# Kernel optimization log

Hardware: AMD Instinct MI355X
Metric: run time of the kernel (lower is better)

## Reference

```python
import jax, jax.numpy as jnp
import numpy as np

N = 50000
E = 1600000
SI, SO, VI, VO, H, SVOD = 128, 128, 16, 16, 16, 3
EPS = 1e-8


def _safe_norm(x, axis, keepdims=False):
    return jnp.sqrt(jnp.sum(x * x, axis=axis, keepdims=keepdims) + EPS)


def setup_inputs() -> dict:
    key = jax.random.key(0)
    ks = jax.random.split(key, 13)

    def lin(k, fan_in, shape):
        b = 1.0 / np.sqrt(fan_in)
        return jax.random.uniform(k, shape, jnp.float32, -b, b)

    merged_dim = H + SI + 3 * SVOD  # 153
    return {
        "s": jax.random.normal(ks[0], (N, SI), jnp.float32),
        "v": jax.random.normal(ks[1], (N, VI, 3), jnp.float32),
        "frames": jax.random.normal(ks[2], (E, 3, 3), jnp.float32),
        "W_vd": lin(ks[3], VI, (VI, H)),            # vector_down (no bias)
        "W_vdf": lin(ks[4], VI, (VI, SVOD)),        # vector_down_frames (no bias)
        "W_so": lin(ks[5], merged_dim, (merged_dim, SO)),  # scalar_out
        "b_so": lin(ks[6], merged_dim, (SO,)),
        "W_vu": lin(ks[7], H, (H, VO)),             # vector_up (no bias)
        "W_vosf": lin(ks[8], SO, (SO, 3 * SVOD)),   # vector_out_scale_frames
        "b_vosf": lin(ks[9], SO, (3 * SVOD,)),
        "W_vuf": lin(ks[10], SVOD, (SVOD, VO)),     # vector_up_frames (no bias)
        "edge_index": jax.random.randint(ks[11], (2, E), 0, N, jnp.int32),
        "node_inputs": 1,
    }


def reference(s, v, frames, W_vd, W_vdf, W_so, b_so, W_vu, W_vosf, b_vosf, W_vuf, edge_index, node_inputs):
    # node_inputs is assumed truthy (node-wise GCP): gather by source node, scatter-mean back.
    row = edge_index[0]
    deg = jax.ops.segment_sum(jnp.ones((E,), s.dtype), row, num_segments=N)
    inv_deg = 1.0 / jnp.maximum(deg, 1.0)

    v_pre = jnp.swapaxes(v, -1, -2)                 # [N, 3, VI]
    vh = v_pre @ W_vd                                # [N, 3, H]
    vnorm = _safe_norm(vh, axis=-2)                  # [N, H]
    vdf = v_pre @ W_vdf                              # [N, 3, SVOD]

    # scalarize: project gathered source-node vectors onto per-edge frames, scatter-mean
    local = jnp.einsum('eij,ejc->eic', frames, vdf[row])       # [E, 3, SVOD]
    local9 = jnp.swapaxes(local, -1, -2).reshape(E, 3 * SVOD)  # [E, 9]
    sh = jax.ops.segment_sum(local9, row, num_segments=N) * inv_deg[:, None]  # [N, 9]

    merged = jnp.concatenate([s, vnorm, sh], axis=-1)          # [N, SI+H+9]
    scalar_rep = merged @ W_so + b_so                           # [N, SO]

    # vector path with frame gate
    vr = jnp.swapaxes(vh @ W_vu, -1, -2)                        # [N, VO, 3]
    gate = jax.nn.sigmoid(scalar_rep) @ W_vosf + b_vosf         # [N, 9]
    # vectorize: expand gate scalars back into vectors via frames, scatter-mean
    g = gate[row].reshape(E, 3, 3)
    gv_e = jnp.einsum('eji,ejk->eik', g, frames)                # [E, 3, 3]
    gv = jax.ops.segment_sum(gv_e, row, num_segments=N) * inv_deg[:, None, None]  # [N, 3, 3]
    gvr = jnp.swapaxes(jnp.swapaxes(gv, -1, -2) @ W_vuf, -1, -2)  # [N, VO, 3]
    vr = vr * jax.nn.sigmoid(_safe_norm(gvr, axis=-1, keepdims=True))

    return jax.nn.relu(scalar_rep), vr
```

## Files before the change

### kernel.cpp

```cpp
#include <hip/hip_runtime.h>

#define N_NODES 50000
#define N_EDGES 1600000
#define NPB     16
#define NCHAIN  16
#define KSTR    168
#define EPSV    1e-8f

typedef float f32x4 __attribute__((ext_vector_type(4)));
typedef short s16x8 __attribute__((ext_vector_type(8)));

struct f4u { float a, b, c, d; };

__device__ __forceinline__ float sigmoidf_(float x) { return 1.0f / (1.0f + __expf(-x)); }
__device__ __forceinline__ short f2bf(float x) {
    unsigned u = __float_as_uint(x);
    unsigned r = (u + 0x7FFFu + ((u >> 16) & 1u)) >> 16;
    return (short)r;
}
__device__ __forceinline__ float bf2f(short h) {
    return __uint_as_float(((unsigned)(unsigned short)h) << 16);
}

__global__ __launch_bounds__(256) void init_kernel(
    const float* __restrict__ W_so, short* __restrict__ WThi, short* __restrict__ WTlo,
    int* __restrict__ p0, int* __restrict__ p1, int mode) {
    int i = blockIdx.x * 256 + threadIdx.x;
    if (i < 128 * 160) {
        int o = i / 160, k = i - o * 160;
        float w = (k < 153) ? W_so[k * 128 + o] : 0.0f;
        short hh = f2bf(w);
        WThi[i] = hh;
        WTlo[i] = f2bf(w - bf2f(hh));
    }
    if (mode == 2) {
        if (i < N_NODES) p0[i] = 0;
        if (i < N_NODES * NCHAIN) p1[i] = -1;
    } else {
        if (i < N_NODES * NCHAIN) p0[i] = -1;
    }
}

__global__ __launch_bounds__(256) void bucket_csr_kernel(
    const int* __restrict__ row,
    const float* __restrict__ frames,
    int* __restrict__ cnt,
    int* __restrict__ head2,
    int* __restrict__ nxt_ovf,
    float* __restrict__ pay,
    int cap) {
    int e = blockIdx.x * 256 + threadIdx.x;
    if (e >= N_EDGES) return;
    int r = row[e];
    int lidx = atomicAdd(&cnt[r], 1);
    if (lidx < cap) {
        const float* f = frames + (size_t)e * 9;
        f4u x = ((const f4u*)f)[0];
        f4u y = ((const f4u*)f)[1];
        float z8 = f[8];
        float* dst = pay + ((size_t)r * cap + lidx) * 12;
        *(float4*)dst       = make_float4(x.a, x.b, x.c, x.d);
        *(float4*)(dst + 4) = make_float4(y.a, y.b, y.c, y.d);
        *(float4*)(dst + 8) = make_float4(z8, 0.0f, 0.0f, 0.0f);
    } else {
        int prev = atomicExch(&head2[r * NCHAIN + (e & (NCHAIN - 1))], e);
        nxt_ovf[e] = prev;
    }
}

__global__ __launch_bounds__(256) void bucket_fat_kernel(
    const int* __restrict__ row,
    const float* __restrict__ frames,
    int* __restrict__ head,
    float* __restrict__ pay) {
    int e = blockIdx.x * 256 + threadIdx.x;
    if (e >= N_EDGES) return;
    int r = row[e];
    int prev = atomicExch(&head[r * NCHAIN + (e & (NCHAIN - 1))], e);
    const float* f = frames + (size_t)e * 9;
    f4u x = ((const f4u*)f)[0];
    f4u y = ((const f4u*)f)[1];
    float z8 = f[8];
    float4* dst = (float4*)(pay + (size_t)e * 16);
    dst[0] = make_float4(x.a, x.b, x.c, x.d);
    dst[1] = make_float4(y.a, y.b, y.c, y.d);
    dst[2] = make_float4(z8, __int_as_float(prev), 0.0f, 0.0f);
}

__global__ __launch_bounds__(256) void bucket_thin_kernel(
    const int* __restrict__ row,
    int* __restrict__ head,
    int* __restrict__ nxt) {
    int e = blockIdx.x * 256 + threadIdx.x;
    if (e >= N_EDGES) return;
    int r = row[e];
    int prev = atomicExch(&head[r * NCHAIN + (e & (NCHAIN - 1))], e);
    nxt[e] = prev;
}

template<int MODE>
__global__ __launch_bounds__(256) void node_kernel(
    const float* __restrict__ s,
    const float* __restrict__ v,
    const float* __restrict__ fr,
    const float* __restrict__ frames_raw,
    const float* __restrict__ W_vd,
    const float* __restrict__ W_vdf,
    const short* __restrict__ WThi,
    const short* __restrict__ WTlo,
    const float* __restrict__ b_so,
    const float* __restrict__ W_vu,
    const float* __restrict__ W_vosf,
    const float* __restrict__ b_vosf,
    const float* __restrict__ W_vuf,
    const int* __restrict__ cnt_or_head,
    const int* __restrict__ head2,
    const int* __restrict__ nxt,
    int cap,
    float* __restrict__ out0,
    float* __restrict__ out1)
{
    __shared__ __align__(16) short AL[2][NPB][KSTR];
    __shared__ float vL[NPB][48];
    __shared__ float vhL[NPB][3][16];
    __shared__ float FbarL[NPB][9];
    __shared__ float gateL[NPB][12];

    float (*sigL)[128] = (float (*)[128])&AL[0][0][0];

    const int t = threadIdx.x;
    const int base = blockIdx.x * NPB;
    const int nn = t >> 4, h = t & 15;
    const int n = base + nn;

    int e0;
    if (MODE == 2) e0 = cnt_or_head[n];
    else           e0 = cnt_or_head[(size_t)n * NCHAIN + h];

#pragma unroll
    for (int r = 0; r < 3; r++) vL[nn][h * 3 + r] = v[(size_t)n * 48 + h * 3 + r];
    {
        const float4* sp4 = (const float4*)(s + (size_t)n * 128 + h * 8);
        float4 s0 = sp4[0], s1 = sp4[1];
        float sv[8] = {s0.x, s0.y, s0.z, s0.w, s1.x, s1.y, s1.z, s1.w};
        s16x8 shi, slo;
#pragma unroll
        for (int j = 0; j < 8; j++) {
            short hh = f2bf(sv[j]);
            shi[j] = hh;
            slo[j] = f2bf(sv[j] - bf2f(hh));
        }
        *(s16x8*)&AL[0][nn][h * 8] = shi;
        *(s16x8*)&AL[1][nn][h * 8] = slo;
    }

    float fs[10];
#pragma unroll
    for (int k = 0; k < 10; k++) fs[k] = 0.f;
    float invdeg;
    {
        if (MODE == 2) {
            const int cn = e0;
            const int lim = cn < cap ? cn : cap;
            for (int slot = h; slot < lim; slot += 16) {
                const float* pp = fr + ((size_t)n * cap + slot) * 12;
                float4 c0 = *(const float4*)pp;
                float4 c1 = *(const float4*)(pp + 4);
                float f8 = pp[8];
                fs[0] += c0.x; fs[1] += c0.y; fs[2] += c0.z; fs[3] += c0.w;
                fs[4] += c1.x; fs[5] += c1.y; fs[6] += c1.z; fs[7] += c1.w;
                fs[8] += f8;
            }
            int e2 = head2[(size_t)n * NCHAIN + h];
            while (e2 >= 0) {
                int en = nxt[e2];
                const float* f = frames_raw + (size_t)e2 * 9;
                f4u x = ((const f4u*)f)[0];
                f4u y = ((const f4u*)f)[1];
                float z8 = f[8];
                fs[0] += x.a; fs[1] += x.b; fs[2] += x.c; fs[3] += x.d;
                fs[4] += y.a; fs[5] += y.b; fs[6] += y.c; fs[7] += y.d;
                fs[8] += z8;
                e2 = en;
            }
#pragma unroll
            for (int m = 1; m < 16; m <<= 1) {
#pragma unroll
                for (int k = 0; k < 9; k++) fs[k] += __shfl_xor(fs[k], m);
            }
            invdeg = 1.0f / fmaxf((float)cn, 1.0f);
        } else if (MODE == 1) {
            int e = e0;
            while (e >= 0) {
                const float4* p = (const float4*)(fr + (size_t)e * 16);
                float4 c2 = p[2];
                float4 c0 = p[0];
                float4 c1 = p[1];
                int en = __float_as_int(c2.y);
                fs[0] += c0.x; fs[1] += c0.y; fs[2] += c0.z; fs[3] += c0.w;
                fs[4] += c1.x; fs[5] += c1.y; fs[6] += c1.z; fs[7] += c1.w;
                fs[8] += c2.x;
                fs[9] += 1.0f;
                e = en;
            }
#pragma unroll
            for (int m = 1; m < 16; m <<= 1) {
#pragma unroll
                for (int k = 0; k < 10; k++) fs[k] += __shfl_xor(fs[k], m);
            }
            invdeg = 1.0f / fmaxf(fs[9], 1.0f);
        } else {
            int e = e0;
            while (e >= 0) {
                int en = nxt[e];
                const float* f = fr + (size_t)e * 9;
                f4u x = ((const f4u*)f)[0];
                f4u y = ((const f4u*)f)[1];
                float z8 = f[8];
                fs[0] += x.a; fs[1] += x.b; fs[2] += x.c; fs[3] += x.d;
                fs[4] += y.a; fs[5] += y.b; fs[6] += y.c; fs[7] += y.d;
                fs[8] += z8;
                fs[9] += 1.0f;
                e = en;
            }
#pragma unroll
            for (int m = 1; m < 16; m <<= 1) {
#pragma unroll
                for (int k = 0; k < 10; k++) fs[k] += __shfl_xor(fs[k], m);
            }
            invdeg = 1.0f / fmaxf(fs[9], 1.0f);
        }
        if (h < 9) FbarL[nn][h] = fs[h] * invdeg;
    }
    __syncthreads();

    {
        float vh0 = 0.f, vh1 = 0.f, vh2 = 0.f;
#pragma unroll
        for (int i = 0; i < 16; i++) {
            float w = W_vd[i * 16 + h];
            vh0 += vL[nn][i * 3 + 0] * w;
            vh1 += vL[nn][i * 3 + 1] * w;
            vh2 += vL[nn][i * 3 + 2] * w;
        }
        vhL[nn][0][h] = vh0; vhL[nn][1][h] = vh1; vhL[nn][2][h] = vh2;
        float vn = sqrtf(vh0 * vh0 + vh1 * vh1 + vh2 * vh2 + EPSV);
        short hh = f2bf(vn);
        AL[0][nn][128 + h] = hh;
        AL[1][nn][128 + h] = f2bf(vn - bf2f(hh));
        if (h < 9) {
            const int c = h / 3, i = h % 3;
            float a = 0.f;
#pragma unroll
            for (int j = 0; j < 3; j++) {
                float vd = 0.f;
#pragma unroll
                for (int ii = 0; ii < 16; ii++) vd += vL[nn][ii * 3 + j] * W_vdf[ii * 3 + c];
                a += (fs[i * 3 + j] * invdeg) * vd;
            }
            short hs = f2bf(a);
            AL[0][nn][144 + h] = hs;
            AL[1][nn][144 + h] = f2bf(a - bf2f(hs));
        } else {
            AL[0][nn][144 + h] = 0;
            AL[1][nn][144 + h] = 0;
        }
    }
    __syncthreads();

    {
        const int w = t >> 6;
        const int lane = t & 63;
        const int quad = lane >> 4;
        const int col = lane & 15;
        const int o0 = w * 32 + col, o1 = o0 + 16;
        f32x4 acc0 = (f32x4){0.f, 0.f, 0.f, 0.f};
        f32x4 acc1 = (f32x4){0.f, 0.f, 0.f, 0.f};
#pragma unroll
        for (int kk = 0; kk < 5; kk++) {
            const int krow = kk * 32 + quad * 8;
            s16x8 ahi = *(const s16x8*)&AL[0][col][krow];
            s16x8 alo = *(const s16x8*)&AL[1][col][krow];
            s16x8 b0h = *(const s16x8*)&WThi[o0 * 160 + krow];
            s16x8 b0l = *(const s16x8*)&WTlo[o0 * 160 + krow];
            s16x8 b1h = *(const s16x8*)&WThi[o1 * 160 + krow];
            s16x8 b1l = *(const s16x8*)&WTlo[o1 * 160 + krow];
            acc0 = __builtin_amdgcn_mfma_f32_16x16x32_bf16(ahi, b0h, acc0, 0, 0, 0);
            acc0 = __builtin_amdgcn_mfma_f32_16x16x32_bf16(ahi, b0l, acc0, 0, 0, 0);
            acc0 = __builtin_amdgcn_mfma_f32_16x16x32_bf16(alo, b0h, acc0, 0, 0, 0);
            acc1 = __builtin_amdgcn_mfma_f32_16x16x32_bf16(ahi, b1h, acc1, 0, 0, 0);
            acc1 = __builtin_amdgcn_mfma_f32_16x16x32_bf16(ahi, b1l, acc1, 0, 0, 0);
            acc1 = __builtin_amdgcn_mfma_f32_16x16x32_bf16(alo, b1h, acc1, 0, 0, 0);
        }
        __syncthreads();
        {
            float b0 = b_so[o0], b1 = b_so[o1];
#pragma unroll
            for (int r = 0; r < 4; r++) {
                int nl = quad * 4 + r;
                float v0 = acc0[r] + b0;
                float v1 = acc1[r] + b1;
                out0[(size_t)(base + nl) * 128 + o0] = fmaxf(v0, 0.0f);
                out0[(size_t)(base + nl) * 128 + o1] = fmaxf(v1, 0.0f);
                sigL[nl][o0] = sigmoidf_(v0);
                sigL[nl][o1] = sigmoidf_(v1);
            }
        }
    }
    __syncthreads();

    {
        const float* sp = &sigL[nn][h * 8];
        float4 s0 = *(const float4*)sp;
        float4 s1 = *(const float4*)(sp + 4);
        float sv[8] = {s0.x, s0.y, s0.z, s0.w, s1.x, s1.y, s1.z, s1.w};
        float p[9];
#pragma unroll
        for (int k = 0; k < 9; k++) p[k] = 0.f;
#pragma unroll
        for (int i = 0; i < 8; i++) {
            int o = h * 8 + i;
#pragma unroll
            for (int k = 0; k < 9; k++) p[k] += sv[i] * W_vosf[o * 9 + k];
        }
#pragma unroll
        for (int m = 1; m < 16; m <<= 1) {
#pragma unroll
            for (int k = 0; k < 9; k++) p[k] += __shfl_xor(p[k], m);
        }
        if (h < 9) gateL[nn][h] = p[h] + b_vosf[h];
    }
    __syncthreads();

    {
        int o = h;
        float gv[9];
#pragma unroll
        for (int i = 0; i < 3; i++)
#pragma unroll
            for (int kk = 0; kk < 3; kk++) {
                float a = 0.f;
#pragma unroll
                for (int j = 0; j < 3; j++) a += gateL[nn][j * 3 + i] * FbarL[nn][j * 3 + kk];
                gv[i * 3 + kk] = a;
            }
        float gvr[3];
#pragma unroll
        for (int kk = 0; kk < 3; kk++) {
            float a = 0.f;
#pragma unroll
            for (int i = 0; i < 3; i++) a += gv[i * 3 + kk] * W_vuf[i * 16 + o];
            gvr[kk] = a;
        }
        float gn2 = sqrtf(gvr[0] * gvr[0] + gvr[1] * gvr[1] + gvr[2] * gvr[2] + EPSV);
        float sg = sigmoidf_(gn2);
#pragma unroll
        for (int c = 0; c < 3; c++) {
            float a = 0.f;
#pragma unroll
            for (int h2 = 0; h2 < 16; h2++) a += vhL[nn][c][h2] * W_vu[h2 * 16 + o];
            out1[(size_t)n * 48 + o * 3 + c] = a * sg;
        }
    }
}

extern "C" void kernel_launch(void* const* d_in, const int* in_sizes, int n_in,
                              void* d_out, int out_size, void* d_ws, size_t ws_size,
                              hipStream_t stream) {
    const float* s      = (const float*)d_in[0];
    const float* v      = (const float*)d_in[1];
    const float* frames = (const float*)d_in[2];
    const float* W_vd   = (const float*)d_in[3];
    const float* W_vdf  = (const float*)d_in[4];
    const float* W_so   = (const float*)d_in[5];
    const float* b_so   = (const float*)d_in[6];
    const float* W_vu   = (const float*)d_in[7];
    const float* W_vosf = (const float*)d_in[8];
    const float* b_vosf = (const float*)d_in[9];
    const float* W_vuf  = (const float*)d_in[10];
    const int* edge_index = (const int*)d_in[11];

    float* out0 = (float*)d_out;
    float* out1 = out0 + (size_t)N_NODES * 128;

    const size_t wt_b    = (size_t)128 * 160 * sizeof(short);
    const size_t cnt_b   = (size_t)N_NODES * sizeof(int);
    const size_t head2_b = (size_t)N_NODES * NCHAIN * sizeof(int);
    const size_t novf_b  = (size_t)N_EDGES * sizeof(int);
    const size_t csr_base = cnt_b + head2_b + 2 * wt_b + novf_b;
    long cap = 0;
    if (ws_size > csr_base)
        cap = (long)((ws_size - csr_base) / ((size_t)N_NODES * 48));
    if (cap > 64) cap = 64;

    const size_t head_b  = (size_t)N_NODES * NCHAIN * sizeof(int);
    const size_t fat_off = head_b + 2 * wt_b;
    const size_t fat_need = fat_off + (size_t)N_EDGES * 64;

    if (cap >= 32) {
        int*   cnt   = (int*)d_ws;
        int*   head2 = (int*)((char*)d_ws + cnt_b);
        short* WThi  = (short*)((char*)d_ws + cnt_b + head2_b);
        short* WTlo  = WThi + 128 * 160;
        int*   novf  = (int*)((char*)d_ws + cnt_b + head2_b + 2 * wt_b);
        float* pay   = (float*)((char*)d_ws + csr_base);
        init_kernel<<<(N_NODES * NCHAIN + 255) / 256, 256, 0, stream>>>(
            W_so, WThi, WTlo, cnt, head2, 2);
        bucket_csr_kernel<<<(N_EDGES + 255) / 256, 256, 0, stream>>>(
            edge_index, frames, cnt, head2, novf, pay, (int)cap);
        node_kernel<2><<<N_NODES / NPB, 256, 0, stream>>>(
            s, v, pay, frames, W_vd, W_vdf, WThi, WTlo, b_so, W_vu, W_vosf, b_vosf, W_vuf,
            cnt, head2, novf, (int)cap, out0, out1);
    } else if (ws_size >= fat_need) {
        int*   head = (int*)d_ws;
        short* WThi = (short*)((char*)d_ws + head_b);
        short* WTlo = WThi + 128 * 160;
        float* pay  = (float*)((char*)d_ws + fat_off);
        init_kernel<<<(N_NODES * NCHAIN + 255) / 256, 256, 0, stream>>>(
            W_so, WThi, WTlo, head, (int*)nullptr, 1);
        bucket_fat_kernel<<<(N_EDGES + 255) / 256, 256, 0, stream>>>(
            edge_index, frames, head, pay);
        node_kernel<1><<<N_NODES / NPB, 256, 0, stream>>>(
            s, v, pay, frames, W_vd, W_vdf, WThi, WTlo, b_so, W_vu, W_vosf, b_vosf, W_vuf,
            head, (const int*)nullptr, (const int*)nullptr, 0, out0, out1);
    } else {
        int*   head = (int*)d_ws;
        short* WThi = (short*)((char*)d_ws + head_b);
        short* WTlo = WThi + 128 * 160;
        int*   nxt  = (int*)((char*)d_ws + fat_off);
        init_kernel<<<(N_NODES * NCHAIN + 255) / 256, 256, 0, stream>>>(
            W_so, WThi, WTlo, head, (int*)nullptr, 1);
        bucket_thin_kernel<<<(N_EDGES + 255) / 256, 256, 0, stream>>>(
            edge_index, head, nxt);
        node_kernel<0><<<N_NODES / NPB, 256, 0, stream>>>(
            s, v, frames, frames, W_vd, W_vdf, WThi, WTlo, b_so, W_vu, W_vosf, b_vosf, W_vuf,
            head, (const int*)nullptr, nxt, 0, out0, out1);
    }
}
```

Before: 307.5 us.

## Bucket edges by 16-node bins instead of per-node CSR slots

Replaces the per-node bucketed payload (cap slots per node) with per-block bins of 16 nodes, where each edge stores its frame plus a local node id. The node kernel then reads its bin in one contiguous sweep across all 256 threads and reduces into shared memory with LDS float atomics. The goal is to cut atomic contention spread, lower per-node padding waste and uneven per-lane load, and get coalesced reads of the payload. In exchange it adds shared-memory atomics (ten per edge) and a bin-overflow linked-list fallback, and summation order becomes nondeterministic.

Measured after the change: 396.4 us. +28.9%, slower.

```diff
diff --git a/kernel.cpp b/kernel.cpp
--- a/kernel.cpp
+++ b/kernel.cpp
@@ -3,6 +3,7 @@
 #define N_NODES 50000
 #define N_EDGES 1600000
 #define NPB     16
+#define NBINS   (N_NODES / NPB)
 #define NCHAIN  16
 #define KSTR    168
 #define EPSV    1e-8f
@@ -33,38 +34,40 @@
         WThi[i] = hh;
         WTlo[i] = f2bf(w - bf2f(hh));
     }
-    if (mode == 2) {
-        if (i < N_NODES) p0[i] = 0;
+    if (mode == 3) {
+        if (i < NBINS) p0[i] = 0;
         if (i < N_NODES * NCHAIN) p1[i] = -1;
     } else {
         if (i < N_NODES * NCHAIN) p0[i] = -1;
     }
 }
 
-__global__ __launch_bounds__(256) void bucket_csr_kernel(
+__global__ __launch_bounds__(256) void bucket_bin_kernel(
     const int* __restrict__ row,
     const float* __restrict__ frames,
-    int* __restrict__ cnt,
+    int* __restrict__ bincnt,
     int* __restrict__ head2,
-    int* __restrict__ nxt_ovf,
+    int* __restrict__ nxt,
     float* __restrict__ pay,
     int cap) {
     int e = blockIdx.x * 256 + threadIdx.x;
     if (e >= N_EDGES) return;
     int r = row[e];
-    int lidx = atomicAdd(&cnt[r], 1);
-    if (lidx < cap) {
-        const float* f = frames + (size_t)e * 9;
-        f4u x = ((const f4u*)f)[0];
-        f4u y = ((const f4u*)f)[1];
-        float z8 = f[8];
-        float* dst = pay + ((size_t)r * cap + lidx) * 12;
-        *(float4*)dst       = make_float4(x.a, x.b, x.c, x.d);
-        *(float4*)(dst + 4) = make_float4(y.a, y.b, y.c, y.d);
-        *(float4*)(dst + 8) = make_float4(z8, 0.0f, 0.0f, 0.0f);
+    int b = r >> 4;
+    int slot = atomicAdd(&bincnt[b], 1);
+    const float* f = frames + (size_t)e * 9;
+    f4u x = ((const f4u*)f)[0];
+    f4u y = ((const f4u*)f)[1];
+    float z8 = f[8];
+    if (slot < cap) {
+        float* dst = pay + ((size_t)b * cap + slot) * 12;
+        ((f4u*)dst)[0] = x;
+        ((f4u*)dst)[1] = y;
+        dst[8] = z8;
+        ((int*)dst)[9] = r & (NPB - 1);
     } else {
         int prev = atomicExch(&head2[r * NCHAIN + (e & (NCHAIN - 1))], e);
-        nxt_ovf[e] = prev;
+        nxt[e] = prev;
     }
 }
 
@@ -98,11 +101,10 @@
     nxt[e] = prev;
 }
 
-template<int MODE>
-__global__ __launch_bounds__(256) void node_kernel(
+__global__ __launch_bounds__(256) void node_bin_kernel(
     const float* __restrict__ s,
     const float* __restrict__ v,
-    const float* __restrict__ fr,
+    const float* __restrict__ pay,
     const float* __restrict__ frames_raw,
     const float* __restrict__ W_vd,
     const float* __restrict__ W_vdf,
@@ -113,7 +115,7 @@
     const float* __restrict__ W_vosf,
     const float* __restrict__ b_vosf,
     const float* __restrict__ W_vuf,
-    const int* __restrict__ cnt_or_head,
+    const int* __restrict__ bincnt,
     const int* __restrict__ head2,
     const int* __restrict__ nxt,
     int cap,
@@ -125,6 +127,7 @@
     __shared__ float vhL[NPB][3][16];
     __shared__ float FbarL[NPB][9];
     __shared__ float gateL[NPB][12];
+    __shared__ float FsumL[NPB][10];
 
     float (*sigL)[128] = (float (*)[128])&AL[0][0][0];
 
@@ -133,10 +136,7 @@
     const int nn = t >> 4, h = t & 15;
     const int n = base + nn;
 
-    int e0;
-    if (MODE == 2) e0 = cnt_or_head[n];
-    else           e0 = cnt_or_head[(size_t)n * NCHAIN + h];
-
+    if (t < NPB * 10) ((float*)FsumL)[t] = 0.0f;
 #pragma unroll
     for (int r = 0; r < 3; r++) vL[nn][h * 3 + r] = v[(size_t)n * 48 + h * 3 + r];
     {
@@ -153,44 +153,235 @@
         *(s16x8*)&AL[0][nn][h * 8] = shi;
         *(s16x8*)&AL[1][nn][h * 8] = slo;
     }
+    __syncthreads();
+
+    {
+        int cn = bincnt[blockIdx.x];
+        int lim = cn < cap ? cn : cap;
+        for (int slot = t; slot < lim; slot += 256) {
+            const float* pp = pay + ((size_t)blockIdx.x * cap + slot) * 12;
+            f4u c0 = ((const f4u*)pp)[0];
+            f4u c1 = ((const f4u*)pp)[1];
+            float f8 = pp[8];
+            int nid = ((const int*)pp)[9];
+            float* Fs = FsumL[nid];
+            atomicAdd(&Fs[0], c0.a); atomicAdd(&Fs[1], c0.b);
+            atomicAdd(&Fs[2], c0.c); atomicAdd(&Fs[3], c0.d);
+            atomicAdd(&Fs[4], c1.a); atomicAdd(&Fs[5], c1.b);
+            atomicAdd(&Fs[6], c1.c); atomicAdd(&Fs[7], c1.d);
+            atomicAdd(&Fs[8], f8);   atomicAdd(&Fs[9], 1.0f);
+        }
+        int e2 = head2[(size_t)n * NCHAIN + h];
+        while (e2 >= 0) {
+            int en = nxt[e2];
+            const float* f = frames_raw + (size_t)e2 * 9;
+            f4u x = ((const f4u*)f)[0];
+            f4u y = ((const f4u*)f)[1];
+            float z8 = f[8];
+            float* Fs = FsumL[nn];
+            atomicAdd(&Fs[0], x.a); atomicAdd(&Fs[1], x.b);
+            atomicAdd(&Fs[2], x.c); atomicAdd(&Fs[3], x.d);
+            atomicAdd(&Fs[4], y.a); atomicAdd(&Fs[5], y.b);
+            atomicAdd(&Fs[6], y.c); atomicAdd(&Fs[7], y.d);
+            atomicAdd(&Fs[8], z8);  atomicAdd(&Fs[9], 1.0f);
+            e2 = en;
+        }
+    }
+    __syncthreads();
+
+    {
+        float fs[10];
+#pragma unroll
+        for (int k = 0; k < 10; k++) fs[k] = FsumL[nn][k];
+        float invdeg = 1.0f / fmaxf(fs[9], 1.0f);
+        if (h < 9) FbarL[nn][h] = fs[h] * invdeg;
+
+        float vh0 = 0.f, vh1 = 0.f, vh2 = 0.f;
+#pragma unroll
+        for (int i = 0; i < 16; i++) {
+            float w = W_vd[i * 16 + h];
+            vh0 += vL[nn][i * 3 + 0] * w;
+            vh1 += vL[nn][i * 3 + 1] * w;
+            vh2 += vL[nn][i * 3 + 2] * w;
+        }
+        vhL[nn][0][h] = vh0; vhL[nn][1][h] = vh1; vhL[nn][2][h] = vh2;
+        float vn = sqrtf(vh0 * vh0 + vh1 * vh1 + vh2 * vh2 + EPSV);
+        short hh = f2bf(vn);
+        AL[0][nn][128 + h] = hh;
+        AL[1][nn][128 + h] = f2bf(vn - bf2f(hh));
+        if (h < 9) {
+            const int c = h / 3, i = h % 3;
+            float a = 0.f;
+#pragma unroll
+            for (int j = 0; j < 3; j++) {
+                float vd = 0.f;
+#pragma unroll
+                for (int ii = 0; ii < 16; ii++) vd += vL[nn][ii * 3 + j] * W_vdf[ii * 3 + c];
+                a += (fs[i * 3 + j] * invdeg) * vd;
+            }
+            short hs = f2bf(a);
+            AL[0][nn][144 + h] = hs;
+            AL[1][nn][144 + h] = f2bf(a - bf2f(hs));
+        } else {
+            AL[0][nn][144 + h] = 0;
+            AL[1][nn][144 + h] = 0;
+        }
+    }
+    __syncthreads();
+
+    {
+        const int w = t >> 6;
+        const int lane = t & 63;
+        const int quad = lane >> 4;
+        const int col = lane & 15;
+        const int o0 = w * 32 + col, o1 = o0 + 16;
+        f32x4 acc0 = (f32x4){0.f, 0.f, 0.f, 0.f};
+        f32x4 acc1 = (f32x4){0.f, 0.f, 0.f, 0.f};
+#pragma unroll
+        for (int kk = 0; kk < 5; kk++) {
+            const int krow = kk * 32 + quad * 8;
+            s16x8 ahi = *(const s16x8*)&AL[0][col][krow];
+            s16x8 alo = *(const s16x8*)&AL[1][col][krow];
+            s16x8 b0h = *(const s16x8*)&WThi[o0 * 160 + krow];
+            s16x8 b0l = *(const s16x8*)&WTlo[o0 * 160 + krow];
+            s16x8 b1h = *(const s16x8*)&WThi[o1 * 160 + krow];
+            s16x8 b1l = *(const s16x8*)&WTlo[o1 * 160 + krow];
+            acc0 = __builtin_amdgcn_mfma_f32_16x16x32_bf16(ahi, b0h, acc0, 0, 0, 0);
+            acc0 = __builtin_amdgcn_mfma_f32_16x16x32_bf16(ahi, b0l, acc0, 0, 0, 0);
+            acc0 = __builtin_amdgcn_mfma_f32_16x16x32_bf16(alo, b0h, acc0, 0, 0, 0);
+            acc1 = __builtin_amdgcn_mfma_f32_16x16x32_bf16(ahi, b1h, acc1, 0, 0, 0);
+            acc1 = __builtin_amdgcn_mfma_f32_16x16x32_bf16(ahi, b1l, acc1, 0, 0, 0);
+            acc1 = __builtin_amdgcn_mfma_f32_16x16x32_bf16(alo, b1h, acc1, 0, 0, 0);
+        }
+        __syncthreads();
+        {
+            float b0 = b_so[o0], b1 = b_so[o1];
+#pragma unroll
+            for (int r = 0; r < 4; r++) {
+                int nl = quad * 4 + r;
+                float v0 = acc0[r] + b0;
+                float v1 = acc1[r] + b1;
+                out0[(size_t)(base + nl) * 128 + o0] = fmaxf(v0, 0.0f);
+                out0[(size_t)(base + nl) * 128 + o1] = fmaxf(v1, 0.0f);
+                sigL[nl][o0] = sigmoidf_(v0);
+                sigL[nl][o1] = sigmoidf_(v1);
+            }
+        }
+    }
+    __syncthreads();
+
+    {
+        const float* sp = &sigL[nn][h * 8];
+        float4 s0 = *(const float4*)sp;
+        float4 s1 = *(const float4*)(sp + 4);
+        float sv[8] = {s0.x, s0.y, s0.z, s0.w, s1.x, s1.y, s1.z, s1.w};
+        float p[9];
+#pragma unroll
+        for (int k = 0; k < 9; k++) p[k] = 0.f;
+#pragma unroll
+        for (int i = 0; i < 8; i++) {
+            int o = h * 8 + i;
+#pragma unroll
+            for (int k = 0; k < 9; k++) p[k] += sv[i] * W_vosf[o * 9 + k];
+        }
+#pragma unroll
+        for (int m = 1; m < 16; m <<= 1) {
+#pragma unroll
+            for (int k = 0; k < 9; k++) p[k] += __shfl_xor(p[k], m);
+        }
+        if (h < 9) gateL[nn][h] = p[h] + b_vosf[h];
+    }
+    __syncthreads();
+
+    {
+        int o = h;
+        float gv[9];
+#pragma unroll
+        for (int i = 0; i < 3; i++)
+#pragma unroll
+            for (int kk = 0; kk < 3; kk++) {
+                float a = 0.f;
+#pragma unroll
+                for (int j = 0; j < 3; j++) a += gateL[nn][j * 3 + i] * FbarL[nn][j * 3 + kk];
+                gv[i * 3 + kk] = a;
+            }
+        float gvr[3];
+#pragma unroll
+        for (int kk = 0; kk < 3; kk++) {
+            float a = 0.f;
+#pragma unroll
+            for (int i = 0; i < 3; i++) a += gv[i * 3 + kk] * W_vuf[i * 16 + o];
+            gvr[kk] = a;
+        }
+        float gn2 = sqrtf(gvr[0] * gvr[0] + gvr[1] * gvr[1] + gvr[2] * gvr[2] + EPSV);
+        float sg = sigmoidf_(gn2);
+#pragma unroll
+        for (int c = 0; c < 3; c++) {
+            float a = 0.f;
+#pragma unroll
+            for (int h2 = 0; h2 < 16; h2++) a += vhL[nn][c][h2] * W_vu[h2 * 16 + o];
+            out1[(size_t)n * 48 + o * 3 + c] = a * sg;
+        }
+    }
+}
+
+template<int MODE>
+__global__ __launch_bounds__(256) void node_kernel(
+    const float* __restrict__ s,
+    const float* __restrict__ v,
+    const float* __restrict__ fr,
+    const float* __restrict__ W_vd,
+    const float* __restrict__ W_vdf,
+    const short* __restrict__ WThi,
+    const short* __restrict__ WTlo,
+    const float* __restrict__ b_so,
+    const float* __restrict__ W_vu,
+    const float* __restrict__ W_vosf,
+    const float* __restrict__ b_vosf,
+    const float* __restrict__ W_vuf,
+    const int* __restrict__ head,
+    const int* __restrict__ nxt,
+    float* __restrict__ out0,
+    float* __restrict__ out1)
+{
+    __shared__ __align__(16) short AL[2][NPB][KSTR];
+    __shared__ float vL[NPB][48];
+    __shared__ float vhL[NPB][3][16];
+    __shared__ float FbarL[NPB][9];
+    __shared__ float gateL[NPB][12];
+
+    float (*sigL)[128] = (float (*)[128])&AL[0][0][0];
+
+    const int t = threadIdx.x;
+    const int base = blockIdx.x * NPB;
+    const int nn = t >> 4, h = t & 15;
+    const int n = base + nn;
+
+    int e = head[(size_t)n * NCHAIN + h];
+
+#pragma unroll
+    for (int r = 0; r < 3; r++) vL[nn][h * 3 + r] = v[(size_t)n * 48 + h * 3 + r];
+    {
+        const float4* sp4 = (const float4*)(s + (size_t)n * 128 + h * 8);
+        float4 s0 = sp4[0], s1 = sp4[1];
+        float sv[8] = {s0.x, s0.y, s0.z, s0.w, s1.x, s1.y, s1.z, s1.w};
+        s16x8 shi, slo;
+#pragma unroll
+        for (int j = 0; j < 8; j++) {
+            short hh = f2bf(sv[j]);
+            shi[j] = hh;
+            slo[j] = f2bf(sv[j] - bf2f(hh));
+        }
+        *(s16x8*)&AL[0][nn][h * 8] = shi;
+        *(s16x8*)&AL[1][nn][h * 8] = slo;
+    }
 
     float fs[10];
 #pragma unroll
     for (int k = 0; k < 10; k++) fs[k] = 0.f;
     float invdeg;
     {
-        if (MODE == 2) {
-            const int cn = e0;
-            const int lim = cn < cap ? cn : cap;
-            for (int slot = h; slot < lim; slot += 16) {
-                const float* pp = fr + ((size_t)n * cap + slot) * 12;
-                float4 c0 = *(const float4*)pp;
-                float4 c1 = *(const float4*)(pp + 4);
-                float f8 = pp[8];
-                fs[0] += c0.x; fs[1] += c0.y; fs[2] += c0.z; fs[3] += c0.w;
-                fs[4] += c1.x; fs[5] += c1.y; fs[6] += c1.z; fs[7] += c1.w;
-                fs[8] += f8;
-            }
-            int e2 = head2[(size_t)n * NCHAIN + h];
-            while (e2 >= 0) {
-                int en = nxt[e2];
-                const float* f = frames_raw + (size_t)e2 * 9;
-                f4u x = ((const f4u*)f)[0];
-                f4u y = ((const f4u*)f)[1];
-                float z8 = f[8];
-                fs[0] += x.a; fs[1] += x.b; fs[2] += x.c; fs[3] += x.d;
-                fs[4] += y.a; fs[5] += y.b; fs[6] += y.c; fs[7] += y.d;
-                fs[8] += z8;
-                e2 = en;
-            }
-#pragma unroll
-            for (int m = 1; m < 16; m <<= 1) {
-#pragma unroll
-                for (int k = 0; k < 9; k++) fs[k] += __shfl_xor(fs[k], m);
-            }
-            invdeg = 1.0f / fmaxf((float)cn, 1.0f);
-        } else if (MODE == 1) {
-            int e = e0;
+        if (MODE == 1) {
             while (e >= 0) {
                 const float4* p = (const float4*)(fr + (size_t)e * 16);
                 float4 c2 = p[2];
@@ -203,14 +394,7 @@
                 fs[9] += 1.0f;
                 e = en;
             }
-#pragma unroll
-            for (int m = 1; m < 16; m <<= 1) {
-#pragma unroll
-                for (int k = 0; k < 10; k++) fs[k] += __shfl_xor(fs[k], m);
-            }
-            invdeg = 1.0f / fmaxf(fs[9], 1.0f);
         } else {
-            int e = e0;
             while (e >= 0) {
                 int en = nxt[e];
                 const float* f = fr + (size_t)e * 9;
@@ -223,13 +407,13 @@
                 fs[9] += 1.0f;
                 e = en;
             }
-#pragma unroll
-            for (int m = 1; m < 16; m <<= 1) {
-#pragma unroll
-                for (int k = 0; k < 10; k++) fs[k] += __shfl_xor(fs[k], m);
-            }
-            invdeg = 1.0f / fmaxf(fs[9], 1.0f);
-        }
+        }
+#pragma unroll
+        for (int m = 1; m < 16; m <<= 1) {
+#pragma unroll
+            for (int k = 0; k < 10; k++) fs[k] += __shfl_xor(fs[k], m);
+        }
+        invdeg = 1.0f / fmaxf(fs[9], 1.0f);
         if (h < 9) FbarL[nn][h] = fs[h] * invdeg;
     }
     __syncthreads();
@@ -384,33 +568,33 @@
     float* out1 = out0 + (size_t)N_NODES * 128;
 
     const size_t wt_b    = (size_t)128 * 160 * sizeof(short);
-    const size_t cnt_b   = (size_t)N_NODES * sizeof(int);
+    const size_t bcnt_b  = (size_t)3136 * sizeof(int);
     const size_t head2_b = (size_t)N_NODES * NCHAIN * sizeof(int);
-    const size_t novf_b  = (size_t)N_EDGES * sizeof(int);
-    const size_t csr_base = cnt_b + head2_b + 2 * wt_b + novf_b;
-    long cap = 0;
-    if (ws_size > csr_base)
-        cap = (long)((ws_size - csr_base) / ((size_t)N_NODES * 48));
-    if (cap > 64) cap = 64;
+    const size_t nxt_b   = (size_t)N_EDGES * sizeof(int);
+    const size_t bin_base = bcnt_b + head2_b + 2 * wt_b + nxt_b;
+    long capB = 0;
+    if (ws_size > bin_base)
+        capB = (long)((ws_size - bin_base) / ((size_t)NBINS * 48));
+    if (capB > 1024) capB = 1024;
 
     const size_t head_b  = (size_t)N_NODES * NCHAIN * sizeof(int);
     const size_t fat_off = head_b + 2 * wt_b;
     const size_t fat_need = fat_off + (size_t)N_EDGES * 64;
 
-    if (cap >= 32) {
-        int*   cnt   = (int*)d_ws;
-        int*   head2 = (int*)((char*)d_ws + cnt_b);
-        short* WThi  = (short*)((char*)d_ws + cnt_b + head2_b);
+    if (capB >= 560) {
+        int*   bcnt  = (int*)d_ws;
+        int*   head2 = (int*)((char*)d_ws + bcnt_b);
+        short* WThi  = (short*)((char*)d_ws + bcnt_b + head2_b);
         short* WTlo  = WThi + 128 * 160;
-        int*   novf  = (int*)((char*)d_ws + cnt_b + head2_b + 2 * wt_b);
-        float* pay   = (float*)((char*)d_ws + csr_base);
+        int*   nxt   = (int*)((char*)d_ws + bcnt_b + head2_b + 2 * wt_b);
+        float* pay   = (float*)((char*)d_ws + bin_base);
         init_kernel<<<(N_NODES * NCHAIN + 255) / 256, 256, 0, stream>>>(
-            W_so, WThi, WTlo, cnt, head2, 2);
-        bucket_csr_kernel<<<(N_EDGES + 255) / 256, 256, 0, stream>>>(
-            edge_index, frames, cnt, head2, novf, pay, (int)cap);
-        node_kernel<2><<<N_NODES / NPB, 256, 0, stream>>>(
+            W_so, WThi, WTlo, bcnt, head2, 3);
+        bucket_bin_kernel<<<(N_EDGES + 255) / 256, 256, 0, stream>>>(
+            edge_index, frames, bcnt, head2, nxt, pay, (int)capB);
+        node_bin_kernel<<<NBINS, 256, 0, stream>>>(
             s, v, pay, frames, W_vd, W_vdf, WThi, WTlo, b_so, W_vu, W_vosf, b_vosf, W_vuf,
-            cnt, head2, novf, (int)cap, out0, out1);
+            bcnt, head2, nxt, (int)capB, out0, out1);
     } else if (ws_size >= fat_need) {
         int*   head = (int*)d_ws;
         short* WThi = (short*)((char*)d_ws + head_b);
@@ -421,19 +605,19 @@
         bucket_fat_kernel<<<(N_EDGES + 255) / 256, 256, 0, stream>>>(
             edge_index, frames, head, pay);
         node_kernel<1><<<N_NODES / NPB, 256, 0, stream>>>(
-            s, v, pay, frames, W_vd, W_vdf, WThi, WTlo, b_so, W_vu, W_vosf, b_vosf, W_vuf,
-            head, (const int*)nullptr, (const int*)nullptr, 0, out0, out1);
+            s, v, pay, W_vd, W_vdf, WThi, WTlo, b_so, W_vu, W_vosf, b_vosf, W_vuf,
+            head, (const int*)nullptr, out0, out1);
     } else {
         int*   head = (int*)d_ws;
         short* WThi = (short*)((char*)d_ws + head_b);
         short* WTlo = WThi + 128 * 160;
         int*   nxt  = (int*)((char*)d_ws + fat_off);
         init_kernel<<<(N_NODES * NCHAIN + 255) / 256, 256, 0, stream>>>(
-            W_so, WThi, WTlo, head, (int*)nullptr, 1);
+            W_so, WThi, WTlo, head, (int*)nullptr, 0);
         bucket_thin_kernel<<<(N_EDGES + 255) / 256, 256, 0, stream>>>(
             edge_index, head, nxt);
         node_kernel<0><<<N_NODES / NPB, 256, 0, stream>>>(
-            s, v, frames, frames, W_vd, W_vdf, WThi, WTlo, b_so, W_vu, W_vosf, b_vosf, W_vuf,
-            head, (const int*)nullptr, nxt, 0, out0, out1);
-    }
-}
+            s, v, frames, W_vd, W_vdf, WThi, WTlo, b_so, W_vu, W_vosf, b_vosf, W_vuf,
+            head, nxt, out0, out1);
+    }
+}
```
